# Optimization experiments

Measured on AMD Instinct MI355X. Metric: run time of the kernel, lower is better.

## Reference

```python
import jax, jax.numpy as jnp
import numpy as np

B, N_L, C, NH = 8, 256, 256, 8
HH, WW = 64, 64
N_C = HH * WW
L = 3  # focal_level
KS = [3, 5, 7]  # focal kernel sizes: focal_factor*k + focal_window
HD = C // NH
SCALE = HD ** -0.5


def _dwconv(x, w, k):
    # x: [B,C,H,W], w: [C,1,k,k] depthwise (groups=C)
    p = k // 2
    return jax.lax.conv_general_dilated(
        x, w, window_strides=(1, 1), padding=[(p, p), (p, p)],
        feature_group_count=C,
        dimension_numbers=('NCHW', 'OIHW', 'NCHW'))


def setup_inputs() -> dict:
    key = jax.random.key(0)
    ks = jax.random.split(key, 16)
    s = 0.02
    inp = {
        'latents': jax.random.normal(ks[0], (B, N_L, C), jnp.float32),
        'context': jax.random.normal(ks[1], (B, N_C, C), jnp.float32),
        'q_w': jax.random.normal(ks[2], (C, C), jnp.float32) * s,
        'k_w': jax.random.normal(ks[3], (C, C), jnp.float32) * s,
        'f_w': jax.random.normal(ks[4], (C + L + 1, C), jnp.float32) * s,
        'f_b': jnp.zeros((C + L + 1,), jnp.float32),
        'h_w': jax.random.normal(ks[5], (C, C), jnp.float32) * s,
        'h_b': jnp.zeros((C,), jnp.float32),
        'fk0': jax.random.normal(ks[6], (C, 1, KS[0], KS[0]), jnp.float32) * s,
        'fk1': jax.random.normal(ks[7], (C, 1, KS[1], KS[1]), jnp.float32) * s,
        'fk2': jax.random.normal(ks[8], (C, 1, KS[2], KS[2]), jnp.float32) * s,
        'proj_w': jax.random.normal(ks[9], (C, C), jnp.float32) * s,
        'proj_b': jnp.zeros((C,), jnp.float32),
        'H': HH,
        'W': WW,
    }
    return inp


def reference(latents, context, q_w, k_w, f_w, f_b, h_w, h_b,
              fk0, fk1, fk2, proj_w, proj_b, H, W):
    gelu = lambda x: jax.nn.gelu(x, approximate=False)
    # attention scores
    q = (latents @ q_w.T).reshape(B, N_L, NH, HD).transpose(0, 2, 1, 3)  # [B,NH,Nl,HD]
    k = (context @ k_w.T).reshape(B, N_C, NH, HD).transpose(0, 2, 1, 3)  # [B,NH,Nc,HD]
    attn = jax.nn.softmax(jnp.einsum('bhnd,bhmd->bhnm', q, k) * SCALE, axis=-1)
    # focal modulation on context
    f_out = context.reshape(B, H, W, C) @ f_w.T + f_b          # [B,H,W,C+L+1]
    f_out = f_out.transpose(0, 3, 1, 2)                        # [B,C+L+1,H,W]
    v_ctx, gates = f_out[:, :C], f_out[:, C:]
    v_ctx_all = jnp.zeros_like(v_ctx)
    for l, fk in enumerate((fk0, fk1, fk2)):
        v_ctx = gelu(_dwconv(v_ctx, fk, KS[l]))
        v_ctx_all = v_ctx_all + v_ctx * gates[:, l:l + 1]
    v_global = gelu(v_ctx.mean(axis=(2, 3), keepdims=True))
    v_ctx_all = v_ctx_all + v_global * gates[:, L:L + 1]
    # 1x1 conv modulator
    v_mod = jnp.einsum('bchw,dc->bdhw', v_ctx_all, h_w) + h_b[None, :, None, None]
    # NOTE: faithful to original -- raw reshape of NCHW tensor (no permute)
    v = v_mod.reshape(B, N_C, NH, HD).transpose(0, 2, 1, 3)    # [B,NH,Nc,HD]
    out = jnp.einsum('bhnm,bhmd->bhnd', attn, v)               # [B,NH,Nl,HD]
    out = out.transpose(0, 2, 1, 3).reshape(B, N_L, C)
    out = out @ proj_w.T + proj_b
    return out, attn
```

## Files before the change

kernel.cpp:

```cpp
#include <hip/hip_runtime.h>
#include <math.h>


namespace {

constexpr float CSCALE = 0.17677669529663688f;

typedef __attribute__((ext_vector_type(8))) __bf16 bf16x8;
typedef __attribute__((ext_vector_type(4))) float f32x4;

__device__ __forceinline__ float gelu_f(float x) {
  return 0.5f * x * (1.0f + erff(x * 0.70710678118654752f));
}

__device__ __forceinline__ unsigned short f2bf(float f) {
  union { float f; unsigned u; } v; v.f = f;
  unsigned r = v.u + 0x7fffu + ((v.u >> 16) & 1u);
  return (unsigned short)(r >> 16);
}

__device__ __forceinline__ float bf2f(unsigned short u) {
  union { unsigned u; float f; } v; v.u = (unsigned)u << 16;
  return v.f;
}

__device__ __forceinline__ bf16x8 pack8(float4 a, float4 b) {
  union { unsigned short u[8]; bf16x8 v; } A;
  A.u[0] = f2bf(a.x); A.u[1] = f2bf(a.y); A.u[2] = f2bf(a.z); A.u[3] = f2bf(a.w);
  A.u[4] = f2bf(b.x); A.u[5] = f2bf(b.y); A.u[6] = f2bf(b.z); A.u[7] = f2bf(b.w);
  return A.v;
}

__global__ __launch_bounds__(256) void cast_w(
    const float* __restrict__ qw, const float* __restrict__ kw,
    const float* __restrict__ fw, const float* __restrict__ hww,
    const float* __restrict__ pw,
    unsigned short* qwb, unsigned short* kwb, unsigned short* fwb,
    unsigned short* hwb, unsigned short* pwb) {
  const int blk = blockIdx.x;
  const float* s; unsigned short* d; int b0, nq;
  if      (blk < 16) { s = qw;  d = qwb; b0 = blk;      nq = 16384; }
  else if (blk < 32) { s = kw;  d = kwb; b0 = blk - 16; nq = 16384; }
  else if (blk < 49) { s = fw;  d = fwb; b0 = blk - 32; nq = 16640; }
  else if (blk < 65) { s = hww; d = hwb; b0 = blk - 49; nq = 16384; }
  else               { s = pw;  d = pwb; b0 = blk - 65; nq = 16384; }
  #pragma unroll
  for (int t = 0; t < 4; ++t) {
    const int q = b0*1024 + t*256 + threadIdx.x;
    if (q < nq) {
      float4 v = ((const float4*)s)[q];
      ushort4 o;
      o.x = f2bf(v.x); o.y = f2bf(v.y); o.z = f2bf(v.z); o.w = f2bf(v.w);
      ((ushort4*)d)[q] = o;
    }
  }
}

__global__ __launch_bounds__(256) void mfma_proj_rw(
    const float* __restrict__ A, const unsigned short* __restrict__ W,
    unsigned short* __restrict__ out) {
  const int r0 = blockIdx.x * 64;
  const int tid = threadIdx.x, w = tid >> 6, l = tid & 63;
  const int lr = l & 15, lk = l >> 4;
  const int rw = r0 + w*16;
  const float* ap = A + (size_t)(rw + lr)*256 + lk*8;
  f32x4 acc[16];
  #pragma unroll
  for (int j = 0; j < 16; ++j) acc[j] = (f32x4){0.f,0.f,0.f,0.f};
  #pragma unroll
  for (int k0 = 0; k0 < 256; k0 += 32) {
    float4 c0 = *(const float4*)(ap + k0);
    float4 c1 = *(const float4*)(ap + k0 + 4);
    bf16x8 a = pack8(c0, c1);
    #pragma unroll
    for (int j = 0; j < 16; ++j) {
      bf16x8 b = *reinterpret_cast<const bf16x8*>(W + (size_t)(j*16 + lr)*256 + k0 + lk*8);
      acc[j] = __builtin_amdgcn_mfma_f32_16x16x32_bf16(a, b, acc[j], 0, 0, 0);
    }
  }
  #pragma unroll
  for (int j = 0; j < 16; ++j)
    #pragma unroll
    for (int rr = 0; rr < 4; ++rr)
      out[(size_t)(rw + lk*4 + rr)*256 + j*16 + lr] = f2bf(acc[j][rr]);
}

__global__ __launch_bounds__(256) void mfma_kproj(
    const float* __restrict__ A, const unsigned short* __restrict__ W,
    unsigned short* __restrict__ kpl) {
  __shared__ unsigned short sh[64 * 264];
  const int r0 = blockIdx.x * 64;
  const int tid = threadIdx.x, w = tid >> 6, l = tid & 63;
  const int lr = l & 15, lk = l >> 4;
  const int rw = r0 + w*16;
  const float* ap = A + (size_t)(rw + lr)*256 + lk*8;
  f32x4 acc[16];
  #pragma unroll
  for (int j = 0; j < 16; ++j) acc[j] = (f32x4){0.f,0.f,0.f,0.f};
  #pragma unroll
  for (int k0 = 0; k0 < 256; k0 += 32) {
    float4 c0 = *(const float4*)(ap + k0);
    float4 c1 = *(const float4*)(ap + k0 + 4);
    bf16x8 a = pack8(c0, c1);
    #pragma unroll
    for (int j = 0; j < 16; ++j) {
      bf16x8 b = *reinterpret_cast<const bf16x8*>(W + (size_t)(j*16 + lr)*256 + k0 + lk*8);
      acc[j] = __builtin_amdgcn_mfma_f32_16x16x32_bf16(a, b, acc[j], 0, 0, 0);
    }
  }
  #pragma unroll
  for (int j = 0; j < 16; ++j)
    #pragma unroll
    for (int rr = 0; rr < 4; ++rr)
      sh[(w*16 + lk*4 + rr)*264 + j*16 + lr] = f2bf(acc[j][rr]);
  __syncthreads();
  const int b = r0 >> 12, mm0 = r0 & 4095;
  #pragma unroll
  for (int it = 0; it < 8; ++it) {
    const int idx = it*256 + tid;
    const int ch = idx & 3, m = (idx >> 2) & 63, h = idx >> 8;
    uint4 v = *(const uint4*)&sh[m*264 + h*32 + ch*8];
    *(uint4*)&kpl[(((size_t)(b*8 + h))*4096 + mm0 + m)*32 + ch*8] = v;
  }
}

__global__ __launch_bounds__(256) void mfma_f(
    const float* __restrict__ A, const unsigned short* __restrict__ W,
    const float* __restrict__ fb, unsigned short* __restrict__ vctx,
    float* __restrict__ gates) {
  __shared__ unsigned short sh[256 * 68];
  const int r0 = blockIdx.x * 64;
  const int tid = threadIdx.x, w = tid >> 6, l = tid & 63;
  const int lr = l & 15, lk = l >> 4;
  const int rw = r0 + w*16;
  const float* ap = A + (size_t)(rw + lr)*256 + lk*8;
  f32x4 acc[17];
  #pragma unroll
  for (int j = 0; j < 17; ++j) acc[j] = (f32x4){0.f,0.f,0.f,0.f};
  #pragma unroll
  for (int k0 = 0; k0 < 256; k0 += 32) {
    float4 c0 = *(const float4*)(ap + k0);
    float4 c1 = *(const float4*)(ap + k0 + 4);
    bf16x8 a = pack8(c0, c1);
    #pragma unroll
    for (int j = 0; j < 17; ++j) {
      const int n = j*16 + lr;
      bf16x8 b = {};
      if (n < 260)
        b = *reinterpret_cast<const bf16x8*>(W + (size_t)n*256 + k0 + lk*8);
      acc[j] = __builtin_amdgcn_mfma_f32_16x16x32_bf16(a, b, acc[j], 0, 0, 0);
    }
  }
  const int hwl = w*16 + lk*4;
  #pragma unroll
  for (int j = 0; j < 16; ++j) {
    const float bb = fb[j*16 + lr];
    #pragma unroll
    for (int rr = 0; rr < 4; ++rr)
      sh[(j*16 + lr)*68 + hwl + rr] = f2bf(acc[j][rr] + bb);
  }
  {
    const int rbase = rw + lk*4;
    const int b = rbase >> 12, hw = rbase & 4095;
    if (lr < 4) {
      const float bb = fb[256 + lr];
      float4 o = make_float4(acc[16][0] + bb, acc[16][1] + bb,
                             acc[16][2] + bb, acc[16][3] + bb);
      *(float4*)&gates[((size_t)(b*4 + lr))*4096 + hw] = o;
    }
  }
  __syncthreads();
  const int b = r0 >> 12, hw0 = r0 & 4095;
  #pragma unroll
  for (int it = 0; it < 8; ++it) {
    const int idx = it*256 + tid;
    const int n = idx >> 3, ch = idx & 7;
    uint4 v = *(const uint4*)&sh[n*68 + ch*8];
    *(uint4*)&vctx[((size_t)(b*256 + n))*4096 + hw0 + ch*8] = v;
  }
}

__global__ __launch_bounds__(256) void fused_conv(
    const unsigned short* in, const float* __restrict__ wk3,
    const float* __restrict__ wk5, const float* __restrict__ wk7,
    const float* __restrict__ gates, unsigned short* out) {
  constexpr int TW = 70;
  __shared__ float A[TW * TW];
  __shared__ float w3[9];
  __shared__ float w5[25];
  __shared__ float w7[49];
  __shared__ float red[4];
  const int tid = threadIdx.x;
  const int b = blockIdx.x >> 8, c = blockIdx.x & 255;
  if (tid < 9)  w3[tid] = wk3[c*9  + tid];
  else if (tid < 34) w5[tid-9]  = wk5[c*25 + tid-9];
  else if (tid < 83) w7[tid-34] = wk7[c*49 + tid-34];
  const unsigned short* ip = in + (size_t)(b*256 + c) * 4096;
  for (int idx = tid; idx < TW*TW; idx += 256) {
    const int ty = idx / TW, tx = idx - ty*TW;
    const int gy = ty - 3, gx = tx - 3;
    A[idx] = (gy >= 0 && gy < 64 && gx >= 0 && gx < 64) ? bf2f(ip[gy*64 + gx]) : 0.0f;
  }
  __syncthreads();
  const int x = tid & 63, ys = (tid >> 6) * 16;
  const float* g0 = gates + (size_t)(b*4 + 0) * 4096;
  const float* g1 = gates + (size_t)(b*4 + 1) * 4096;
  const float* g2 = gates + (size_t)(b*4 + 2) * 4096;
  const float* g3 = gates + (size_t)(b*4 + 3) * 4096;
  float s[16], acc[16];
  #pragma unroll
  for (int i = 0; i < 16; ++i) s[i] = 0.f;
  #pragma unroll
  for (int kx = 0; kx < 3; ++kx) {
    const float* col = &A[(ys + 2)*TW + x + 2 + kx];
    #pragma unroll
    for (int r = 0; r < 18; ++r) {
      const float v = col[r*TW];
      #pragma unroll
      for (int ky = 0; ky < 3; ++ky) {
        const int i = r - ky;
        if (i >= 0 && i < 16) s[i] += w3[ky*3 + kx] * v;
      }
    }
  }
  #pragma unroll
  for (int i = 0; i < 16; ++i) {
    s[i] = gelu_f(s[i]);
    acc[i] = s[i] * g0[(ys + i)*64 + x];
  }
  __syncthreads();
  #pragma unroll
  for (int i = 0; i < 16; ++i) A[(ys + i + 3)*TW + x + 3] = s[i];
  __syncthreads();
  #pragma unroll
  for (int i = 0; i < 16; ++i) s[i] = 0.f;
  #pragma unroll
  for (int kx = 0; kx < 5; ++kx) {
    const float* col = &A[(ys + 1)*TW + x + 1 + kx];
    #pragma unroll
    for (int r = 0; r < 20; ++r) {
      const float v = col[r*TW];
      #pragma unroll
      for (int ky = 0; ky < 5; ++ky) {
        const int i = r - ky;
        if (i >= 0 && i < 16) s[i] += w5[ky*5 + kx] * v;
      }
    }
  }
  #pragma unroll
  for (int i = 0; i < 16; ++i) {
    s[i] = gelu_f(s[i]);
    acc[i] += s[i] * g1[(ys + i)*64 + x];
  }
  __syncthreads();
  #pragma unroll
  for (int i = 0; i < 16; ++i) A[(ys + i + 3)*TW + x + 3] = s[i];
  __syncthreads();
  #pragma unroll
  for (int i = 0; i < 16; ++i) s[i] = 0.f;
  #pragma unroll
  for (int kx = 0; kx < 7; ++kx) {
    const float* col = &A[ys*TW + x + kx];
    #pragma unroll
    for (int r = 0; r < 22; ++r) {
      const float v = col[r*TW];
      #pragma unroll
      for (int ky = 0; ky < 7; ++ky) {
        const int i = r - ky;
        if (i >= 0 && i < 16) s[i] += w7[ky*7 + kx] * v;
      }
    }
  }
  float msum = 0.f;
  #pragma unroll
  for (int i = 0; i < 16; ++i) {
    s[i] = gelu_f(s[i]);
    acc[i] += s[i] * g2[(ys + i)*64 + x];
    msum += s[i];
  }
  #pragma unroll
  for (int off = 32; off >= 1; off >>= 1) msum += __shfl_xor(msum, off, 64);
  if ((tid & 63) == 0) red[tid >> 6] = msum;
  __syncthreads();
  const float vg = gelu_f((red[0]+red[1]+red[2]+red[3]) * (1.0f/4096.0f));
  unsigned short* vp = out + (size_t)(b*256 + c) * 4096;
  #pragma unroll
  for (int i = 0; i < 16; ++i) {
    const int pix = (ys + i)*64 + x;
    vp[pix] = f2bf(acc[i] + vg * g3[pix]);
  }
}

__global__ __launch_bounds__(256) void mfma_h(
    const unsigned short* __restrict__ vall, const unsigned short* __restrict__ hwb,
    const float* __restrict__ hb, unsigned short* __restrict__ vlin) {
  __shared__ unsigned short sh[256 * 72];
  const int hw0 = blockIdx.x * 64, b = blockIdx.y;
  const int tid = threadIdx.x, w = tid >> 6, l = tid & 63;
  const int lr = l & 15, lk = l >> 4;
  const int cl = tid >> 3, hl = (tid & 7) * 8;
  #pragma unroll
  for (int c0 = 0; c0 < 256; c0 += 32) {
    const unsigned short* sp = vall + (size_t)(b*256 + c0 + cl)*4096 + hw0 + hl;
    ushort4 u0 = *(const ushort4*)sp;
    ushort4 u1 = *(const ushort4*)(sp + 4);
    sh[(hl+0)*264 + c0+cl] = u0.x; sh[(hl+1)*264 + c0+cl] = u0.y;
    sh[(hl+2)*264 + c0+cl] = u0.z; sh[(hl+3)*264 + c0+cl] = u0.w;
    sh[(hl+4)*264 + c0+cl] = u1.x; sh[(hl+5)*264 + c0+cl] = u1.y;
    sh[(hl+6)*264 + c0+cl] = u1.z; sh[(hl+7)*264 + c0+cl] = u1.w;
  }
  __syncthreads();
  const int dw = w * 64;
  f32x4 acc[4][4];
  #pragma unroll
  for (int j2 = 0; j2 < 4; ++j2)
    #pragma unroll
    for (int j = 0; j < 4; ++j) acc[j2][j] = (f32x4){0.f,0.f,0.f,0.f};
  #pragma unroll
  for (int k0 = 0; k0 < 256; k0 += 32) {
    bf16x8 a[4];
    #pragma unroll
    for (int j2 = 0; j2 < 4; ++j2)
      a[j2] = *reinterpret_cast<const bf16x8*>(hwb + (size_t)(dw + j2*16 + lr)*256 + k0 + lk*8);
    #pragma unroll
    for (int j = 0; j < 4; ++j) {
      bf16x8 bv = *reinterpret_cast<const bf16x8*>(&sh[(j*16 + lr)*264 + k0 + lk*8]);
      #pragma unroll
      for (int j2 = 0; j2 < 4; ++j2)
        acc[j2][j] = __builtin_amdgcn_mfma_f32_16x16x32_bf16(a[j2], bv, acc[j2][j], 0, 0, 0);
    }
  }
  float hbv[4][4];
  #pragma unroll
  for (int j2 = 0; j2 < 4; ++j2)
    #pragma unroll
    for (int rr = 0; rr < 4; ++rr) hbv[j2][rr] = hb[dw + j2*16 + lk*4 + rr];
  __syncthreads();
  #pragma unroll
  for (int j2 = 0; j2 < 4; ++j2)
    #pragma unroll
    for (int j = 0; j < 4; ++j)
      #pragma unroll
      for (int rr = 0; rr < 4; ++rr)
        sh[(dw + j2*16 + lk*4 + rr)*72 + j*16 + lr] = f2bf(acc[j2][j][rr] + hbv[j2][rr]);
  __syncthreads();
  const int q = hw0 >> 8, dim0 = hw0 & 255;
  #pragma unroll
  for (int it = 0; it < 8; ++it) {
    const int dl = it*32 + (tid >> 3);
    const int ch = tid & 7;
    const int m = dl*16 + q;
    uint4 v = *(const uint4*)&sh[dl*72 + ch*8];
    *(uint4*)&vlin[((size_t)(b*4096 + m))*256 + dim0 + ch*8] = v;
  }
}

__global__ __launch_bounds__(256) void trans_bf(
    const unsigned short* __restrict__ vlin, unsigned short* __restrict__ vt) {
  __shared__ unsigned short T[64][72];
  const int tid = threadIdx.x;
  const int m0 = blockIdx.x * 64, d0 = blockIdx.y * 64, b = blockIdx.z;
  #pragma unroll
  for (int it = 0; it < 2; ++it) {
    const int ml = it*32 + (tid >> 3);
    const int ch = tid & 7;
    uint4 v = *(const uint4*)&vlin[((size_t)(b*4096 + m0 + ml))*256 + d0 + ch*8];
    *(uint4*)&T[ml][ch*8] = v;
  }
  __syncthreads();
  #pragma unroll
  for (int it = 0; it < 2; ++it) {
    const int dl = it*32 + (tid >> 3);
    const int ch = tid & 7;
    unsigned short tmp[8];
    #pragma unroll
    for (int k = 0; k < 8; ++k) tmp[k] = T[ch*8 + k][dl];
    *(uint4*)&vt[((size_t)(b*256 + d0 + dl))*4096 + m0 + ch*8] = *(uint4*)tmp;
  }
}

__global__ __launch_bounds__(256) void attn_pv(
    const unsigned short* __restrict__ qb, const unsigned short* __restrict__ kpl,
    const unsigned short* __restrict__ vt, float* __restrict__ attn,
    unsigned short* __restrict__ aout) {
  const int blk = blockIdx.x;
  const int bh = blk & 63, nt = blk >> 6;
  const int b = bh >> 3, h = bh & 7;
  const int tid = threadIdx.x;
  const int w = tid >> 6, l = tid & 63;
  const int lr = l & 15, lk = l >> 4;
  const int n0 = nt * 16;
  __shared__ float rs[4][16];
  __shared__ unsigned short pl[4][16][40];
  __shared__ float ps[4][16][36];
  __shared__ float osum[4][16][32];
  bf16x8 aq = *reinterpret_cast<const bf16x8*>(
      qb + ((size_t)(b*256 + n0 + lr))*256 + h*32 + lk*8);
  const unsigned short* kbase = kpl + ((size_t)(b*8 + h))*4096*32 + lk*8;
  float sum[4] = {0.f, 0.f, 0.f, 0.f};
  #pragma unroll 2
  for (int mt = 0; mt < 64; ++mt) {
    const int m0 = w*1024 + mt*16;
    bf16x8 bk = *reinterpret_cast<const bf16x8*>(kbase + (size_t)(m0 + lr)*32);
    f32x4 d = __builtin_amdgcn_mfma_f32_16x16x32_bf16(aq, bk, (f32x4){0.f,0.f,0.f,0.f}, 0, 0, 0);
    #pragma unroll
    for (int r = 0; r < 4; ++r) sum[r] += __expf(d[r] * CSCALE);
  }
  #pragma unroll
  for (int r = 0; r < 4; ++r) {
    #pragma unroll
    for (int m = 1; m < 16; m <<= 1) sum[r] += __shfl_xor(sum[r], m, 64);
  }
  if (lr == 0) {
    #pragma unroll
    for (int r = 0; r < 4; ++r) rs[w][lk*4 + r] = sum[r];
  }
  __syncthreads();
  float invS[4];
  #pragma unroll
  for (int r = 0; r < 4; ++r) {
    const int rowi = lk*4 + r;
    invS[r] = 1.0f / (rs[0][rowi] + rs[1][rowi] + rs[2][rowi] + rs[3][rowi]);
  }
  float* ab = attn + ((size_t)bh*256 + n0) * 4096;
  const unsigned short* vb = vt + ((size_t)(b*256 + h*32))*4096;
  const int fr = l >> 3;
  const int fm = (l & 7) * 4;
  f32x4 acc0 = {0.f,0.f,0.f,0.f}, acc1 = {0.f,0.f,0.f,0.f};
  for (int mt = 0; mt < 64; ++mt) {
    const int m0 = w*1024 + mt*16;
    bf16x8 bk = *reinterpret_cast<const bf16x8*>(kbase + (size_t)(m0 + lr)*32);
    f32x4 d = __builtin_amdgcn_mfma_f32_16x16x32_bf16(aq, bk, (f32x4){0.f,0.f,0.f,0.f}, 0, 0, 0);
    const int mo = (mt & 1) << 4;
    #pragma unroll
    for (int r = 0; r < 4; ++r) {
      const float p = __expf(d[r] * CSCALE) * invS[r];
      ps[w][lk*4 + r][mo + lr] = p;
      pl[w][lk*4 + r][mo + lr] = f2bf(p);
    }
    if (mt & 1) {
      const int mb = w*1024 + (mt - 1)*16;
      bf16x8 pa = *reinterpret_cast<const bf16x8*>(&pl[w][lr][lk*8]);
      bf16x8 bv0 = *reinterpret_cast<const bf16x8*>(vb + (size_t)lr*4096 + mb + lk*8);
      bf16x8 bv1 = *reinterpret_cast<const bf16x8*>(vb + (size_t)(16 + lr)*4096 + mb + lk*8);
      acc0 = __builtin_amdgcn_mfma_f32_16x16x32_bf16(pa, bv0, acc0, 0, 0, 0);
      acc1 = __builtin_amdgcn_mfma_f32_16x16x32_bf16(pa, bv1, acc1, 0, 0, 0);
      #pragma unroll
      for (int i = 0; i < 2; ++i) {
        const int row = i*8 + fr;
        f32x4 pv4 = *(const f32x4*)&ps[w][row][fm];
        __builtin_nontemporal_store(pv4, (f32x4*)&ab[(size_t)row*4096 + mb + fm]);
      }
    }
  }
  #pragma unroll
  for (int r = 0; r < 4; ++r) {
    osum[w][lk*4 + r][lr]      = acc0[r];
    osum[w][lk*4 + r][16 + lr] = acc1[r];
  }
  __syncthreads();
  for (int i = tid; i < 512; i += 256) {
    const int n = i >> 5, d = i & 31;
    const float s = osum[0][n][d] + osum[1][n][d] + osum[2][n][d] + osum[3][n][d];
    aout[((size_t)(b*256 + n0 + n))*256 + h*32 + d] = f2bf(s);
  }
}

__global__ __launch_bounds__(256) void mfma_proj(
    const unsigned short* __restrict__ A, const unsigned short* __restrict__ W,
    const float* __restrict__ pb, float* __restrict__ out) {
  const int r0 = blockIdx.x * 64, n0 = blockIdx.y * 64;
  const int tid = threadIdx.x, w = tid >> 6, l = tid & 63;
  const int lr = l & 15, lk = l >> 4;
  const int rw = r0 + w*16;
  const unsigned short* ap = A + (size_t)(rw + lr)*256 + lk*8;
  f32x4 acc[4] = {{0.f,0.f,0.f,0.f},{0.f,0.f,0.f,0.f},{0.f,0.f,0.f,0.f},{0.f,0.f,0.f,0.f}};
  #pragma unroll
  for (int k0 = 0; k0 < 256; k0 += 32) {
    bf16x8 a = *reinterpret_cast<const bf16x8*>(ap + k0);
    #pragma unroll
    for (int j = 0; j < 4; ++j) {
      bf16x8 b = *reinterpret_cast<const bf16x8*>(W + (size_t)(n0 + j*16 + lr)*256 + k0 + lk*8);
      acc[j] = __builtin_amdgcn_mfma_f32_16x16x32_bf16(a, b, acc[j], 0, 0, 0);
    }
  }
  #pragma unroll
  for (int j = 0; j < 4; ++j) {
    const int n = n0 + j*16 + lr;
    const float bb = pb[n];
    #pragma unroll
    for (int rr = 0; rr < 4; ++rr)
      out[(size_t)(rw + lk*4 + rr)*256 + n] = acc[j][rr] + bb;
  }
}

}

extern "C" void kernel_launch(void* const* d_in, const int* in_sizes, int n_in,
                              void* d_out, int out_size, void* d_ws, size_t ws_size,
                              hipStream_t stream) {
  (void)in_sizes; (void)n_in; (void)out_size; (void)ws_size;
  const float* latents = (const float*)d_in[0];
  const float* context = (const float*)d_in[1];
  const float* q_w    = (const float*)d_in[2];
  const float* k_w    = (const float*)d_in[3];
  const float* f_w    = (const float*)d_in[4];
  const float* f_b    = (const float*)d_in[5];
  const float* h_w    = (const float*)d_in[6];
  const float* h_b    = (const float*)d_in[7];
  const float* fk0    = (const float*)d_in[8];
  const float* fk1    = (const float*)d_in[9];
  const float* fk2    = (const float*)d_in[10];
  const float* proj_w = (const float*)d_in[11];
  const float* proj_b = (const float*)d_in[12];

  float* out0 = (float*)d_out;
  float* attn = out0 + (size_t)8*256*256;

  char* w = (char*)d_ws;
  unsigned short* vcv     = (unsigned short*)(w + 0x0);
  unsigned short* kpl     = (unsigned short*)(w + 0x1000000);
  unsigned short* v_tb    = (unsigned short*)(w + 0x2000000);
  unsigned short* vlin_bf = (unsigned short*)(w + 0x3000000);
  unsigned short* q_bf    = (unsigned short*)(w + 0x4000000);
  unsigned short* aout_bf = (unsigned short*)(w + 0x4100000);
  unsigned short* qw_bf   = (unsigned short*)(w + 0x4200000);
  unsigned short* kw_bf   = (unsigned short*)(w + 0x4220000);
  unsigned short* fw_bf   = (unsigned short*)(w + 0x4240000);
  unsigned short* hw_bf   = (unsigned short*)(w + 0x4270000);
  unsigned short* pw_bf   = (unsigned short*)(w + 0x4290000);
  float*          gates   = (float*)(w + 0x42B0000);

  cast_w<<<81, 256, 0, stream>>>(q_w, k_w, f_w, h_w, proj_w,
                                 qw_bf, kw_bf, fw_bf, hw_bf, pw_bf);
  mfma_proj_rw<<<32,  256, 0, stream>>>(latents, qw_bf, q_bf);
  mfma_kproj  <<<512, 256, 0, stream>>>(context, kw_bf, kpl);
  mfma_f      <<<512, 256, 0, stream>>>(context, fw_bf, f_b, vcv, gates);
  fused_conv  <<<2048, 256, 0, stream>>>(vcv, fk0, fk1, fk2, gates, vcv);
  mfma_h      <<<dim3(64, 8), 256, 0, stream>>>(vcv, hw_bf, h_b, vlin_bf);
  trans_bf    <<<dim3(64, 4, 8), 256, 0, stream>>>(vlin_bf, v_tb);
  attn_pv     <<<1024, 256, 0, stream>>>(q_bf, kpl, v_tb, attn, aout_bf);
  mfma_proj   <<<dim3(32, 4), 256, 0, stream>>>(aout_bf, pw_bf, proj_b, out0);
}
```

Baseline: 362.7 us.

## Fuse q/k/f projections into one launch and drop weight cast kernel

Removes the separate weight-cast kernel and converts fp32 weights to bf16 on the fly inside each GEMM's fragment load. Also merges the q, k and f projection GEMMs into a single launch that dispatches on block index. The aim is to cut launch overhead and the extra pass over the weights, and to let the three projections overlap on the GPU. In exchange, weight fragments are read as fp32, twice the bytes, and repacked in every block. The fused kernel also reserves the larger shared buffer for all blocks, which can lower occupancy.

Measured after the change: 423.0 us. 16.6% more time.

```diff
diff --git a/kernel.cpp b/kernel.cpp
--- a/kernel.cpp
+++ b/kernel.cpp
@@ -31,152 +31,116 @@
   return A.v;
 }
 
-__global__ __launch_bounds__(256) void cast_w(
+__device__ __forceinline__ bf16x8 wfrag(const float* __restrict__ W,
+                                        int n, int k0, int lk) {
+  const float* p = W + (size_t)n*256 + k0 + lk*8;
+  return pack8(*(const float4*)p, *(const float4*)(p + 4));
+}
+
+__global__ __launch_bounds__(256) void fused_qkf(
+    const float* __restrict__ lat, const float* __restrict__ ctx,
     const float* __restrict__ qw, const float* __restrict__ kw,
-    const float* __restrict__ fw, const float* __restrict__ hww,
-    const float* __restrict__ pw,
-    unsigned short* qwb, unsigned short* kwb, unsigned short* fwb,
-    unsigned short* hwb, unsigned short* pwb) {
+    const float* __restrict__ fw, const float* __restrict__ fb,
+    unsigned short* __restrict__ q_bf, unsigned short* __restrict__ kpl,
+    unsigned short* __restrict__ vctx, float* __restrict__ gates) {
+  __shared__ unsigned short sh[256 * 68];
   const int blk = blockIdx.x;
-  const float* s; unsigned short* d; int b0, nq;
-  if      (blk < 16) { s = qw;  d = qwb; b0 = blk;      nq = 16384; }
-  else if (blk < 32) { s = kw;  d = kwb; b0 = blk - 16; nq = 16384; }
-  else if (blk < 49) { s = fw;  d = fwb; b0 = blk - 32; nq = 16640; }
-  else if (blk < 65) { s = hww; d = hwb; b0 = blk - 49; nq = 16384; }
-  else               { s = pw;  d = pwb; b0 = blk - 65; nq = 16384; }
-  #pragma unroll
-  for (int t = 0; t < 4; ++t) {
-    const int q = b0*1024 + t*256 + threadIdx.x;
-    if (q < nq) {
-      float4 v = ((const float4*)s)[q];
-      ushort4 o;
-      o.x = f2bf(v.x); o.y = f2bf(v.y); o.z = f2bf(v.z); o.w = f2bf(v.w);
-      ((ushort4*)d)[q] = o;
-    }
-  }
-}
-
-__global__ __launch_bounds__(256) void mfma_proj_rw(
-    const float* __restrict__ A, const unsigned short* __restrict__ W,
-    unsigned short* __restrict__ out) {
-  const int r0 = blockIdx.x * 64;
   const int tid = threadIdx.x, w = tid >> 6, l = tid & 63;
   const int lr = l & 15, lk = l >> 4;
-  const int rw = r0 + w*16;
-  const float* ap = A + (size_t)(rw + lr)*256 + lk*8;
-  f32x4 acc[16];
-  #pragma unroll
-  for (int j = 0; j < 16; ++j) acc[j] = (f32x4){0.f,0.f,0.f,0.f};
-  #pragma unroll
-  for (int k0 = 0; k0 < 256; k0 += 32) {
-    float4 c0 = *(const float4*)(ap + k0);
-    float4 c1 = *(const float4*)(ap + k0 + 4);
-    bf16x8 a = pack8(c0, c1);
+
+  if (blk < 32) {
+    const int r0 = blk * 64, rw = r0 + w*16;
+    const float* ap = lat + (size_t)(rw + lr)*256 + lk*8;
+    f32x4 acc[16];
+    #pragma unroll
+    for (int j = 0; j < 16; ++j) acc[j] = (f32x4){0.f,0.f,0.f,0.f};
+    #pragma unroll
+    for (int k0 = 0; k0 < 256; k0 += 32) {
+      bf16x8 a = pack8(*(const float4*)(ap + k0), *(const float4*)(ap + k0 + 4));
+      #pragma unroll
+      for (int j = 0; j < 16; ++j) {
+        bf16x8 b = wfrag(qw, j*16 + lr, k0, lk);
+        acc[j] = __builtin_amdgcn_mfma_f32_16x16x32_bf16(a, b, acc[j], 0, 0, 0);
+      }
+    }
+    #pragma unroll
+    for (int j = 0; j < 16; ++j)
+      #pragma unroll
+      for (int rr = 0; rr < 4; ++rr)
+        q_bf[(size_t)(rw + lk*4 + rr)*256 + j*16 + lr] = f2bf(acc[j][rr]);
+  } else if (blk < 544) {
+    const int r0 = (blk - 32) * 64, rw = r0 + w*16;
+    const float* ap = ctx + (size_t)(rw + lr)*256 + lk*8;
+    f32x4 acc[16];
+    #pragma unroll
+    for (int j = 0; j < 16; ++j) acc[j] = (f32x4){0.f,0.f,0.f,0.f};
+    #pragma unroll
+    for (int k0 = 0; k0 < 256; k0 += 32) {
+      bf16x8 a = pack8(*(const float4*)(ap + k0), *(const float4*)(ap + k0 + 4));
+      #pragma unroll
+      for (int j = 0; j < 16; ++j) {
+        bf16x8 b = wfrag(kw, j*16 + lr, k0, lk);
+        acc[j] = __builtin_amdgcn_mfma_f32_16x16x32_bf16(a, b, acc[j], 0, 0, 0);
+      }
+    }
+    #pragma unroll
+    for (int j = 0; j < 16; ++j)
+      #pragma unroll
+      for (int rr = 0; rr < 4; ++rr)
+        sh[(w*16 + lk*4 + rr)*264 + j*16 + lr] = f2bf(acc[j][rr]);
+    __syncthreads();
+    const int b = r0 >> 12, mm0 = r0 & 4095;
+    #pragma unroll
+    for (int it = 0; it < 8; ++it) {
+      const int idx = it*256 + tid;
+      const int ch = idx & 3, m = (idx >> 2) & 63, h = idx >> 8;
+      uint4 v = *(const uint4*)&sh[m*264 + h*32 + ch*8];
+      *(uint4*)&kpl[(((size_t)(b*8 + h))*4096 + mm0 + m)*32 + ch*8] = v;
+    }
+  } else {
+    const int r0 = (blk - 544) * 64, rw = r0 + w*16;
+    const float* ap = ctx + (size_t)(rw + lr)*256 + lk*8;
+    f32x4 acc[17];
+    #pragma unroll
+    for (int j = 0; j < 17; ++j) acc[j] = (f32x4){0.f,0.f,0.f,0.f};
+    #pragma unroll
+    for (int k0 = 0; k0 < 256; k0 += 32) {
+      bf16x8 a = pack8(*(const float4*)(ap + k0), *(const float4*)(ap + k0 + 4));
+      #pragma unroll
+      for (int j = 0; j < 17; ++j) {
+        const int n = j*16 + lr;
+        bf16x8 b = {};
+        if (n < 260) b = wfrag(fw, n, k0, lk);
+        acc[j] = __builtin_amdgcn_mfma_f32_16x16x32_bf16(a, b, acc[j], 0, 0, 0);
+      }
+    }
+    const int hwl = w*16 + lk*4;
     #pragma unroll
     for (int j = 0; j < 16; ++j) {
-      bf16x8 b = *reinterpret_cast<const bf16x8*>(W + (size_t)(j*16 + lr)*256 + k0 + lk*8);
-      acc[j] = __builtin_amdgcn_mfma_f32_16x16x32_bf16(a, b, acc[j], 0, 0, 0);
-    }
-  }
-  #pragma unroll
-  for (int j = 0; j < 16; ++j)
-    #pragma unroll
-    for (int rr = 0; rr < 4; ++rr)
-      out[(size_t)(rw + lk*4 + rr)*256 + j*16 + lr] = f2bf(acc[j][rr]);
-}
-
-__global__ __launch_bounds__(256) void mfma_kproj(
-    const float* __restrict__ A, const unsigned short* __restrict__ W,
-    unsigned short* __restrict__ kpl) {
-  __shared__ unsigned short sh[64 * 264];
-  const int r0 = blockIdx.x * 64;
-  const int tid = threadIdx.x, w = tid >> 6, l = tid & 63;
-  const int lr = l & 15, lk = l >> 4;
-  const int rw = r0 + w*16;
-  const float* ap = A + (size_t)(rw + lr)*256 + lk*8;
-  f32x4 acc[16];
-  #pragma unroll
-  for (int j = 0; j < 16; ++j) acc[j] = (f32x4){0.f,0.f,0.f,0.f};
-  #pragma unroll
-  for (int k0 = 0; k0 < 256; k0 += 32) {
-    float4 c0 = *(const float4*)(ap + k0);
-    float4 c1 = *(const float4*)(ap + k0 + 4);
-    bf16x8 a = pack8(c0, c1);
-    #pragma unroll
-    for (int j = 0; j < 16; ++j) {
-      bf16x8 b = *reinterpret_cast<const bf16x8*>(W + (size_t)(j*16 + lr)*256 + k0 + lk*8);
-      acc[j] = __builtin_amdgcn_mfma_f32_16x16x32_bf16(a, b, acc[j], 0, 0, 0);
-    }
-  }
-  #pragma unroll
-  for (int j = 0; j < 16; ++j)
-    #pragma unroll
-    for (int rr = 0; rr < 4; ++rr)
-      sh[(w*16 + lk*4 + rr)*264 + j*16 + lr] = f2bf(acc[j][rr]);
-  __syncthreads();
-  const int b = r0 >> 12, mm0 = r0 & 4095;
-  #pragma unroll
-  for (int it = 0; it < 8; ++it) {
-    const int idx = it*256 + tid;
-    const int ch = idx & 3, m = (idx >> 2) & 63, h = idx >> 8;
-    uint4 v = *(const uint4*)&sh[m*264 + h*32 + ch*8];
-    *(uint4*)&kpl[(((size_t)(b*8 + h))*4096 + mm0 + m)*32 + ch*8] = v;
-  }
-}
-
-__global__ __launch_bounds__(256) void mfma_f(
-    const float* __restrict__ A, const unsigned short* __restrict__ W,
-    const float* __restrict__ fb, unsigned short* __restrict__ vctx,
-    float* __restrict__ gates) {
-  __shared__ unsigned short sh[256 * 68];
-  const int r0 = blockIdx.x * 64;
-  const int tid = threadIdx.x, w = tid >> 6, l = tid & 63;
-  const int lr = l & 15, lk = l >> 4;
-  const int rw = r0 + w*16;
-  const float* ap = A + (size_t)(rw + lr)*256 + lk*8;
-  f32x4 acc[17];
-  #pragma unroll
-  for (int j = 0; j < 17; ++j) acc[j] = (f32x4){0.f,0.f,0.f,0.f};
-  #pragma unroll
-  for (int k0 = 0; k0 < 256; k0 += 32) {
-    float4 c0 = *(const float4*)(ap + k0);
-    float4 c1 = *(const float4*)(ap + k0 + 4);
-    bf16x8 a = pack8(c0, c1);
-    #pragma unroll
-    for (int j = 0; j < 17; ++j) {
-      const int n = j*16 + lr;
-      bf16x8 b = {};
-      if (n < 260)
-        b = *reinterpret_cast<const bf16x8*>(W + (size_t)n*256 + k0 + lk*8);
-      acc[j] = __builtin_amdgcn_mfma_f32_16x16x32_bf16(a, b, acc[j], 0, 0, 0);
-    }
-  }
-  const int hwl = w*16 + lk*4;
-  #pragma unroll
-  for (int j = 0; j < 16; ++j) {
-    const float bb = fb[j*16 + lr];
-    #pragma unroll
-    for (int rr = 0; rr < 4; ++rr)
-      sh[(j*16 + lr)*68 + hwl + rr] = f2bf(acc[j][rr] + bb);
-  }
-  {
-    const int rbase = rw + lk*4;
-    const int b = rbase >> 12, hw = rbase & 4095;
-    if (lr < 4) {
-      const float bb = fb[256 + lr];
-      float4 o = make_float4(acc[16][0] + bb, acc[16][1] + bb,
-                             acc[16][2] + bb, acc[16][3] + bb);
-      *(float4*)&gates[((size_t)(b*4 + lr))*4096 + hw] = o;
-    }
-  }
-  __syncthreads();
-  const int b = r0 >> 12, hw0 = r0 & 4095;
-  #pragma unroll
-  for (int it = 0; it < 8; ++it) {
-    const int idx = it*256 + tid;
-    const int n = idx >> 3, ch = idx & 7;
-    uint4 v = *(const uint4*)&sh[n*68 + ch*8];
-    *(uint4*)&vctx[((size_t)(b*256 + n))*4096 + hw0 + ch*8] = v;
+      const float bb = fb[j*16 + lr];
+      #pragma unroll
+      for (int rr = 0; rr < 4; ++rr)
+        sh[(j*16 + lr)*68 + hwl + rr] = f2bf(acc[j][rr] + bb);
+    }
+    {
+      const int rbase = rw + lk*4;
+      const int b = rbase >> 12, hw = rbase & 4095;
+      if (lr < 4) {
+        const float bb = fb[256 + lr];
+        float4 o = make_float4(acc[16][0] + bb, acc[16][1] + bb,
+                               acc[16][2] + bb, acc[16][3] + bb);
+        *(float4*)&gates[((size_t)(b*4 + lr))*4096 + hw] = o;
+      }
+    }
+    __syncthreads();
+    const int b = r0 >> 12, hw0 = r0 & 4095;
+    #pragma unroll
+    for (int it = 0; it < 8; ++it) {
+      const int idx = it*256 + tid;
+      const int n = idx >> 3, ch = idx & 7;
+      uint4 v = *(const uint4*)&sh[n*68 + ch*8];
+      *(uint4*)&vctx[((size_t)(b*256 + n))*4096 + hw0 + ch*8] = v;
+    }
   }
 }
 
@@ -292,7 +256,7 @@
 }
 
 __global__ __launch_bounds__(256) void mfma_h(
-    const unsigned short* __restrict__ vall, const unsigned short* __restrict__ hwb,
+    const unsigned short* __restrict__ vall, const float* __restrict__ hww,
     const float* __restrict__ hb, unsigned short* __restrict__ vlin) {
   __shared__ unsigned short sh[256 * 72];
   const int hw0 = blockIdx.x * 64, b = blockIdx.y;
@@ -321,7 +285,7 @@
     bf16x8 a[4];
     #pragma unroll
     for (int j2 = 0; j2 < 4; ++j2)
-      a[j2] = *reinterpret_cast<const bf16x8*>(hwb + (size_t)(dw + j2*16 + lr)*256 + k0 + lk*8);
+      a[j2] = wfrag(hww, dw + j2*16 + lr, k0, lk);
     #pragma unroll
     for (int j = 0; j < 4; ++j) {
       bf16x8 bv = *reinterpret_cast<const bf16x8*>(&sh[(j*16 + lr)*264 + k0 + lk*8]);
@@ -467,7 +431,7 @@
 }
 
 __global__ __launch_bounds__(256) void mfma_proj(
-    const unsigned short* __restrict__ A, const unsigned short* __restrict__ W,
+    const unsigned short* __restrict__ A, const float* __restrict__ W,
     const float* __restrict__ pb, float* __restrict__ out) {
   const int r0 = blockIdx.x * 64, n0 = blockIdx.y * 64;
   const int tid = threadIdx.x, w = tid >> 6, l = tid & 63;
@@ -480,7 +444,7 @@
     bf16x8 a = *reinterpret_cast<const bf16x8*>(ap + k0);
     #pragma unroll
     for (int j = 0; j < 4; ++j) {
-      bf16x8 b = *reinterpret_cast<const bf16x8*>(W + (size_t)(n0 + j*16 + lr)*256 + k0 + lk*8);
+      bf16x8 b = wfrag(W, n0 + j*16 + lr, k0, lk);
       acc[j] = __builtin_amdgcn_mfma_f32_16x16x32_bf16(a, b, acc[j], 0, 0, 0);
     }
   }
@@ -524,21 +488,13 @@
   unsigned short* vlin_bf = (unsigned short*)(w + 0x3000000);
   unsigned short* q_bf    = (unsigned short*)(w + 0x4000000);
   unsigned short* aout_bf = (unsigned short*)(w + 0x4100000);
-  unsigned short* qw_bf   = (unsigned short*)(w + 0x4200000);
-  unsigned short* kw_bf   = (unsigned short*)(w + 0x4220000);
-  unsigned short* fw_bf   = (unsigned short*)(w + 0x4240000);
-  unsigned short* hw_bf   = (unsigned short*)(w + 0x4270000);
-  unsigned short* pw_bf   = (unsigned short*)(w + 0x4290000);
-  float*          gates   = (float*)(w + 0x42B0000);
-
-  cast_w<<<81, 256, 0, stream>>>(q_w, k_w, f_w, h_w, proj_w,
-                                 qw_bf, kw_bf, fw_bf, hw_bf, pw_bf);
-  mfma_proj_rw<<<32,  256, 0, stream>>>(latents, qw_bf, q_bf);
-  mfma_kproj  <<<512, 256, 0, stream>>>(context, kw_bf, kpl);
-  mfma_f      <<<512, 256, 0, stream>>>(context, fw_bf, f_b, vcv, gates);
-  fused_conv  <<<2048, 256, 0, stream>>>(vcv, fk0, fk1, fk2, gates, vcv);
-  mfma_h      <<<dim3(64, 8), 256, 0, stream>>>(vcv, hw_bf, h_b, vlin_bf);
-  trans_bf    <<<dim3(64, 4, 8), 256, 0, stream>>>(vlin_bf, v_tb);
-  attn_pv     <<<1024, 256, 0, stream>>>(q_bf, kpl, v_tb, attn, aout_bf);
-  mfma_proj   <<<dim3(32, 4), 256, 0, stream>>>(aout_bf, pw_bf, proj_b, out0);
-}
+  float*          gates   = (float*)(w + 0x4200000);
+
+  fused_qkf <<<1056, 256, 0, stream>>>(latents, context, q_w, k_w, f_w, f_b,
+                                       q_bf, kpl, vcv, gates);
+  fused_conv<<<2048, 256, 0, stream>>>(vcv, fk0, fk1, fk2, gates, vcv);
+  mfma_h    <<<dim3(64, 8), 256, 0, stream>>>(vcv, h_w, h_b, vlin_bf);
+  trans_bf  <<<dim3(64, 4, 8), 256, 0, stream>>>(vlin_bf, v_tb);
+  attn_pv   <<<1024, 256, 0, stream>>>(q_bf, kpl, v_tb, attn, aout_bf);
+  mfma_proj <<<dim3(32, 4), 256, 0, stream>>>(aout_bf, proj_w, proj_b, out0);
+}
```
